# Kernel tuning notes

Hardware: AMD Instinct MI355X
Metric: run time of the kernel (lower is better)

The kernel has to match this reference:

```python
import jax, jax.numpy as jnp
import numpy as np
import math

N_HEAD = 16
N_HEAD_KV = 4
HEAD_DIM = 128
N_EMBD = 2048

def alibi_slopes(n_heads):
    def pow2_slopes(n):
        start = 2 ** (-2 ** (-(math.log2(n) - 3)))
        return [start * start ** i for i in range(n)]
    if math.log2(n_heads).is_integer():
        return jnp.array(pow2_slopes(n_heads), dtype=jnp.float32)
    closest = 2 ** math.floor(math.log2(n_heads))
    base = pow2_slopes(closest)
    if n_heads <= 2 * closest:
        s = base + base[0::2]
    else:
        s = base + base[0::2] + base[1::2]
    return jnp.array(s[:n_heads], dtype=jnp.float32)

def setup_inputs() -> dict:
    key = jax.random.key(0)
    ks = jax.random.split(key, 5)
    B, T, C = 2, 2048, N_EMBD
    kvdim = N_HEAD_KV * HEAD_DIM
    sc = 0.02
    return {
        "x": jax.random.normal(ks[0], (B, T, C), dtype=jnp.float32),
        "q_w": jax.random.normal(ks[1], (C, C), dtype=jnp.float32) * sc,
        "k_w": jax.random.normal(ks[2], (kvdim, C), dtype=jnp.float32) * sc,
        "v_w": jax.random.normal(ks[3], (kvdim, C), dtype=jnp.float32) * sc,
        "o_w": jax.random.normal(ks[4], (C, C), dtype=jnp.float32) * sc,
    }

def reference(x, q_w, k_w, v_w, o_w):
    B, T, C = x.shape
    H, Hkv, D = N_HEAD, N_HEAD_KV, HEAD_DIM
    # nan/inf sanitize (no-op for random inputs, kept for fidelity)
    x = jnp.nan_to_num(x, nan=0.0, posinf=10000.0, neginf=-10000.0)
    q = (x @ q_w.T).reshape(B, T, H, D).transpose(0, 2, 1, 3)      # [B,H,T,D]
    k = (x @ k_w.T).reshape(B, T, Hkv, D).transpose(0, 2, 1, 3)    # [B,Hkv,T,D]
    v = (x @ v_w.T).reshape(B, T, Hkv, D).transpose(0, 2, 1, 3)
    # repeat_interleave KV heads to H heads
    rep = H // Hkv
    k = jnp.repeat(k, rep, axis=1)
    v = jnp.repeat(v, rep, axis=1)
    scale = 1.0 / math.sqrt(D)
    att = jnp.einsum('bhqd,bhkd->bhqk', q, k) * scale
    att = jnp.clip(att, -10000.0, 10000.0)
    pos = jnp.arange(T)
    causal = jnp.where(pos[None, :] > pos[:, None], -jnp.inf, 0.0)  # [T,T]
    slopes = alibi_slopes(H)  # [H]
    rel = (pos[None, :] - pos[:, None]).astype(jnp.float32)         # [T,T]
    alibi = slopes[:, None, None] * rel[None]                        # [H,T,T]
    att = att + causal[None, None] + alibi[None]
    att = jax.nn.softmax(att.astype(jnp.float32), axis=-1).astype(q.dtype)
    y = jnp.einsum('bhqk,bhkd->bhqd', att, v)
    y = jnp.nan_to_num(y, nan=0.0, posinf=10000.0, neginf=-10000.0)
    y = y.transpose(0, 2, 1, 3).reshape(B, T, C)
    return y @ o_w.T
```

## Files before the change

kernel.cpp:

```cpp
#include <hip/hip_runtime.h>
#include <hip/hip_bf16.h>
#include <math.h>

#define SEQ   2048
#define EMBD  2048
#define NH    16
#define NKV   4
#define HD    128
#define NQKV  3072

typedef __attribute__((ext_vector_type(8))) short short8;
typedef __attribute__((ext_vector_type(4))) short short4v;
typedef __attribute__((ext_vector_type(4))) float floatx4;

static __device__ __forceinline__ short f2bf(float f) {
    union { float f; unsigned u; } cv; cv.f = f;
    unsigned u = cv.u;
    u += 0x7FFF + ((u >> 16) & 1);
    return (short)(u >> 16);
}

#define GL16(gsrc, ldst)                                                        \
    __builtin_amdgcn_global_load_lds(                                           \
        (const __attribute__((address_space(1))) void*)(gsrc),                  \
        (__attribute__((address_space(3))) void*)(ldst), 16, 0, 0)

static __device__ __forceinline__ int alibi_window(float slope2) {
    return (int)ceilf((42.0f / slope2 + 63.0f) * (1.0f / 64.0f));
}

__global__ void cvt_all(const float* __restrict__ x,  const float* __restrict__ qw,
                        const float* __restrict__ kw, const float* __restrict__ vw,
                        const float* __restrict__ ow,
                        short* __restrict__ xb, short* __restrict__ wall,
                        short* __restrict__ owb) {
    int i = blockIdx.x * blockDim.x + threadIdx.x;
    const float* src; short* dst; int off;
    if (i < 2097152)      { src = x;  dst = xb;             off = i; }
    else if (i < 3145728) { src = qw; dst = wall;           off = i - 2097152; }
    else if (i < 3407872) { src = kw; dst = wall + 4194304; off = i - 3145728; }
    else if (i < 3670016) { src = vw; dst = wall + 5242880; off = i - 3407872; }
    else                  { src = ow; dst = owb;            off = i - 3670016; }
    float4 v = ((const float4*)src)[off];
    float a[4] = {v.x, v.y, v.z, v.w};
    short4v o;
#pragma unroll
    for (int j = 0; j < 4; ++j) {
        float f = a[j];
        f = isnan(f) ? 0.0f : fminf(fmaxf(f, -10000.0f), 10000.0f);
        o[j] = f2bf(f);
    }
    ((short4v*)dst)[off] = o;
}

template<int MODE>
__global__ __launch_bounds__(256) void gemm_bt(
    const short* __restrict__ A, const short* __restrict__ W,
    float* __restrict__ Cout, int M, int N, int K,
    short* __restrict__ qb, short* __restrict__ kb, short* __restrict__ vb)
{
    __shared__ __align__(16) short sA[128 * 32];
    __shared__ __align__(16) short sB[128 * 32];

    const int tid  = threadIdx.x;
    const int lane = tid & 63;
    const int wv   = tid >> 6;
    const int wr   = wv >> 1, wc = wv & 1;
    const int lr   = lane & 15, lg = lane >> 4;
    const int bn   = blockIdx.x, bm = blockIdx.y;

    const short* gA[2]; const short* gB[2];
    short* lA[2]; short* lB[2];
#pragma unroll
    for (int s = 0; s < 2; ++s) {
        int chunk = wv * 128 + s * 64 + lane;
        int row = chunk >> 2, seg = chunk & 3;
        gA[s] = A + (size_t)(bm * 128 + row) * K + seg * 8;
        gB[s] = W + (size_t)(bn * 128 + row) * K + seg * 8;
        lA[s] = &sA[(wv * 128 + s * 64) * 8];
        lB[s] = &sB[(wv * 128 + s * 64) * 8];
    }

    floatx4 acc[4][4] = {};
    const int nkt = K / 32;
    for (int kt = 0; kt < nkt; ++kt) {
#pragma unroll
        for (int s = 0; s < 2; ++s) {
            GL16(gA[s] + kt * 32, lA[s]);
            GL16(gB[s] + kt * 32, lB[s]);
        }
        __syncthreads();

        short8 af[4], bfr[4];
#pragma unroll
        for (int i = 0; i < 4; ++i) {
            af[i]  = *(const short8*)&sA[(wr * 64 + i * 16 + lr) * 32 + lg * 8];
            bfr[i] = *(const short8*)&sB[(wc * 64 + i * 16 + lr) * 32 + lg * 8];
        }
#pragma unroll
        for (int i = 0; i < 4; ++i)
#pragma unroll
            for (int j = 0; j < 4; ++j)
                acc[i][j] = __builtin_amdgcn_mfma_f32_16x16x32_bf16(af[i], bfr[j], acc[i][j], 0, 0, 0);
        __syncthreads();
    }

    const float QSCALE = 0.08838834764831845f * 1.44269504f;
#pragma unroll
    for (int i = 0; i < 4; ++i)
#pragma unroll
        for (int j = 0; j < 4; ++j)
#pragma unroll
            for (int r = 0; r < 4; ++r) {
                int gm = bm * 128 + wr * 64 + i * 16 + lg * 4 + r;
                int gn = bn * 128 + wc * 64 + j * 16 + lr;
                float v = acc[i][j][r];
                if (MODE == 0) {
                    int b = gm >> 11, t = gm & (SEQ - 1);
                    if (gn < 2048) {
                        int h = gn >> 7, d = gn & 127;
                        qb[(((size_t)(b * NH + h)) * SEQ + t) * HD + d] = f2bf(v * QSCALE);
                    } else if (gn < 2560) {
                        int hk = (gn - 2048) >> 7, d = gn & 127;
                        kb[(((size_t)(b * NKV + hk)) * SEQ + t) * HD + d] = f2bf(v);
                    } else {
                        int hv = (gn - 2560) >> 7, d = gn & 127;
                        vb[(((size_t)(b * NKV + hv)) * HD + d) * SEQ + t] = f2bf(v);
                    }
                } else {
                    Cout[(size_t)gm * N + gn] = v;
                }
            }
}

__global__ __launch_bounds__(512, 4) void attn_fwd(
    const short* __restrict__ Q, const short* __restrict__ Kg,
    const short* __restrict__ VT, short* __restrict__ Y)
{
    __shared__ __align__(16) short sK[2][64 * 128];
    __shared__ __align__(16) short sV[128 * 64];
    __shared__ short Plds[8][16][72];

    const int tid  = threadIdx.x;
    const int wave = tid >> 6, lane = tid & 63;
    const int lr = lane & 15, lg = lane >> 4;
    const int bid = blockIdx.x;

    const int u = (bid & 1) ? (511 - (bid >> 1)) : (bid >> 1);
    const int p = u & 15, h = (u >> 4) & 15, b = u >> 8;
    const int hkv = h >> 2;
    const int qgw = 2 * p + (wave < 4 ? 1 : 0);

    const short* Qb = Q  +  ((size_t)(b * NH  + h  )) * SEQ * HD;
    const short* Kp = Kg +  ((size_t)(b * NKV + hkv)) * SEQ * HD;
    const short* Vp = VT +  ((size_t)(b * NKV + hkv)) * HD * SEQ;

    const float slope2 = exp2f(-0.5f * (float)(h + 1)) * 1.44269504f;
    const int W = alibi_window(slope2);
    const int thi = 2 * p + 1;
    int tlo = thi - W; if (tlo < 0) tlo = 0;

    const short* gK[2]; const short* gV[2];
    int lOff[2];
#pragma unroll
    for (int j = 0; j < 2; ++j) {
        int ck = wave * 128 + j * 64 + lane;
        int krow = ck >> 4, kseg = ck & 15;
        gK[j] = Kp + (size_t)krow * HD + (kseg ^ (krow & 7)) * 8;
        int vrow = ck >> 3, vseg = ck & 7;
        gV[j] = Vp + (size_t)vrow * SEQ + (vseg ^ (vrow & 7)) * 8;
        lOff[j] = (wave * 128 + j * 64) * 8;
    }

    float c_nt[4];
#pragma unroll
    for (int nt = 0; nt < 4; ++nt) c_nt[nt] = slope2 * (float)(nt * 16 + lr);

    const int q0 = qgw * 64 + (wave & 3) * 16;
    short8 qf[4];
#pragma unroll
    for (int cc = 0; cc < 4; ++cc)
        qf[cc] = *(const short8*)&Qb[(size_t)(q0 + lr) * HD + cc * 32 + lg * 8];

    floatx4 po[8] = {};
    float m[4], lsum[4];
#pragma unroll
    for (int r = 0; r < 4; ++r) { m[r] = -3.0e38f; lsum[r] = 0.0f; }

    int cur = 0;
#pragma unroll
    for (int j = 0; j < 2; ++j)
        GL16(gK[j] + (size_t)(thi << 6) * HD, &sK[0][0] + lOff[j]);
    __syncthreads();

#pragma unroll 1
    for (int t = thi; t >= tlo; --t) {
#pragma unroll
        for (int j = 0; j < 2; ++j)
            GL16(gV[j] + (t << 6), &sV[0] + lOff[j]);
        if (t > tlo) {
#pragma unroll
            for (int j = 0; j < 2; ++j)
                GL16(gK[j] + (size_t)((t - 1) << 6) * HD, &sK[cur ^ 1][0] + lOff[j]);
        }

        const bool active = (t <= qgw) && (t > qgw - W);
        const int kv0 = t << 6;

        if (active) {
            const short* kr = &sK[cur][0];
            floatx4 sf[4];
#pragma unroll
            for (int nt = 0; nt < 4; ++nt) {
                floatx4 sacc = {0.f, 0.f, 0.f, 0.f};
#pragma unroll
                for (int cc = 0; cc < 4; ++cc) {
                    int krow = nt * 16 + lr;
                    short8 kf = *(const short8*)&kr[krow * 128 + (((cc * 4 + lg) ^ (krow & 7)) * 8)];
                    sacc = __builtin_amdgcn_mfma_f32_16x16x32_bf16(qf[cc], kf, sacc, 0, 0, 0);
                }
                sf[nt] = sacc;
            }

            const float a2t = slope2 * (float)kv0;
            const bool masked = (t == qgw);
#pragma unroll
            for (int r = 0; r < 4; ++r) {
                const int qpos = q0 + lg * 4 + r;
                float sv[4];
#pragma unroll
                for (int nt = 0; nt < 4; ++nt)
                    sv[nt] = sf[nt][r] + a2t + c_nt[nt];
                if (masked) {
#pragma unroll
                    for (int nt = 0; nt < 4; ++nt) {
                        int kpos = kv0 + nt * 16 + lr;
                        if (kpos > qpos) sv[nt] = -3.0e38f;
                    }
                }
                bool over = (sv[0] > m[r]) | (sv[1] > m[r]) | (sv[2] > m[r]) | (sv[3] > m[r]);
                if (__any(over)) {
                    float mx = fmaxf(fmaxf(sv[0], sv[1]), fmaxf(sv[2], sv[3]));
#pragma unroll
                    for (int off = 1; off < 16; off <<= 1) mx = fmaxf(mx, __shfl_xor(mx, off));
                    float mn = fmaxf(m[r], mx);
                    float rs = exp2f(m[r] - mn);
                    lsum[r] *= rs;
#pragma unroll
                    for (int dt = 0; dt < 8; ++dt) po[dt][r] *= rs;
                    m[r] = mn;
                }
#pragma unroll
                for (int nt = 0; nt < 4; ++nt) {
                    float pp = exp2f(sv[nt] - m[r]);
                    lsum[r] += pp;
                    Plds[wave][lg * 4 + r][nt * 16 + lr] = f2bf(pp);
                }
            }
        }

        __syncthreads();

        if (active) {
            short8 pf0 = *(const short8*)&Plds[wave][lr][lg * 8];
            short8 pf1 = *(const short8*)&Plds[wave][lr][32 + lg * 8];
#pragma unroll
            for (int dt = 0; dt < 8; ++dt) {
                int vrow = dt * 16 + lr;
                short8 vf0 = *(const short8*)&sV[vrow * 64 + (((lg    ) ^ (vrow & 7)) * 8)];
                short8 vf1 = *(const short8*)&sV[vrow * 64 + (((lg + 4) ^ (vrow & 7)) * 8)];
                po[dt] = __builtin_amdgcn_mfma_f32_16x16x32_bf16(pf0, vf0, po[dt], 0, 0, 0);
                po[dt] = __builtin_amdgcn_mfma_f32_16x16x32_bf16(pf1, vf1, po[dt], 0, 0, 0);
            }
        }

        __syncthreads();
        cur ^= 1;
    }

#pragma unroll
    for (int r = 0; r < 4; ++r) {
        float sum = lsum[r];
#pragma unroll
        for (int off = 1; off < 16; off <<= 1) sum += __shfl_xor(sum, off);
        float inv = 1.0f / sum;
        int row = q0 + lg * 4 + r;
#pragma unroll
        for (int dt = 0; dt < 8; ++dt)
            Y[((size_t)(b * SEQ + row)) * EMBD + h * HD + dt * 16 + lr] = f2bf(po[dt][r] * inv);
    }
}

extern "C" void kernel_launch(void* const* d_in, const int* in_sizes, int n_in,
                              void* d_out, int out_size, void* d_ws, size_t ws_size,
                              hipStream_t stream) {
    const float* x   = (const float*)d_in[0];
    const float* q_w = (const float*)d_in[1];
    const float* k_w = (const float*)d_in[2];
    const float* v_w = (const float*)d_in[3];
    const float* o_w = (const float*)d_in[4];
    float* out = (float*)d_out;

    char* ws = (char*)d_ws;
    short* x_bf  = (short*)(ws);
    short* w_all = (short*)(ws + 16777216);
    short* o_wb  = (short*)(ws + 29360128);
    short* q_b   = (short*)(ws + 37748736);
    short* k_b   = (short*)(ws + 54525952);
    short* vT_b  = (short*)(ws + 58720256);
    short* y_b   = (short*)(ws + 62914560);

    cvt_all<<<18432, 256, 0, stream>>>(x, q_w, k_w, v_w, o_w, x_bf, w_all, o_wb);

    gemm_bt<0><<<dim3(NQKV / 128, 4096 / 128), 256, 0, stream>>>(
        x_bf, w_all, nullptr, 4096, NQKV, EMBD, q_b, k_b, vT_b);

    attn_fwd<<<512, 512, 0, stream>>>(q_b, k_b, vT_b, y_b);

    gemm_bt<1><<<dim3(EMBD / 128, 4096 / 128), 256, 0, stream>>>(
        y_b, o_wb, out, 4096, EMBD, EMBD, nullptr, nullptr, nullptr);
}
```

Measured before the change: 238.8 us.

## Double-buffer V tiles and replace full syncs with vmcnt-based waits

V tiles now get a second LDS buffer and are prefetched one iteration ahead together with K. The loop waits on outstanding global-to-LDS loads with explicit s_waitcnt vmcnt counts and raw s_barrier instead of __syncthreads. The P tile in LDS is XOR-swizzled with no padding, and the mid-loop barrier between softmax and PV is removed, since each wave only reads its own P slice. This adds LDS use, which may lower occupancy, and relies on hand-counted vmcnt values being correct.

```diff
diff --git a/kernel.cpp b/kernel.cpp
--- a/kernel.cpp
+++ b/kernel.cpp
@@ -138,8 +138,8 @@
     const short* __restrict__ VT, short* __restrict__ Y)
 {
     __shared__ __align__(16) short sK[2][64 * 128];
-    __shared__ __align__(16) short sV[128 * 64];
-    __shared__ short Plds[8][16][72];
+    __shared__ __align__(16) short sV[2][128 * 64];
+    __shared__ short Plds[8][16][64];
 
     const int tid  = threadIdx.x;
     const int wave = tid >> 6, lane = tid & 63;
@@ -181,6 +181,9 @@
 #pragma unroll
     for (int cc = 0; cc < 4; ++cc)
         qf[cc] = *(const short8*)&Qb[(size_t)(q0 + lr) * HD + cc * 32 + lg * 8];
+#pragma unroll
+    for (int cc = 0; cc < 4; ++cc)
+        asm volatile("" :: "v"(qf[cc]));
 
     floatx4 po[8] = {};
     float m[4], lsum[4];
@@ -189,20 +192,24 @@
 
     int cur = 0;
 #pragma unroll
-    for (int j = 0; j < 2; ++j)
+    for (int j = 0; j < 2; ++j) {
+        GL16(gV[j] + (thi << 6), &sV[0][0] + lOff[j]);
         GL16(gK[j] + (size_t)(thi << 6) * HD, &sK[0][0] + lOff[j]);
-    __syncthreads();
+    }
 
 #pragma unroll 1
     for (int t = thi; t >= tlo; --t) {
-#pragma unroll
-        for (int j = 0; j < 2; ++j)
-            GL16(gV[j] + (t << 6), &sV[0] + lOff[j]);
         if (t > tlo) {
 #pragma unroll
-            for (int j = 0; j < 2; ++j)
+            for (int j = 0; j < 2; ++j) {
+                GL16(gV[j] + ((t - 1) << 6), &sV[cur ^ 1][0] + lOff[j]);
                 GL16(gK[j] + (size_t)((t - 1) << 6) * HD, &sK[cur ^ 1][0] + lOff[j]);
+            }
+            asm volatile("s_waitcnt vmcnt(4)" ::: "memory");
+        } else {
+            asm volatile("s_waitcnt vmcnt(0)" ::: "memory");
         }
+        __builtin_amdgcn_s_barrier();
 
         const bool active = (t <= qgw) && (t > qgw - W);
         const int kv0 = t << 6;
@@ -227,6 +234,7 @@
 #pragma unroll
             for (int r = 0; r < 4; ++r) {
                 const int qpos = q0 + lg * 4 + r;
+                const int row = lg * 4 + r;
                 float sv[4];
 #pragma unroll
                 for (int nt = 0; nt < 4; ++nt)
@@ -254,27 +262,24 @@
                 for (int nt = 0; nt < 4; ++nt) {
                     float pp = exp2f(sv[nt] - m[r]);
                     lsum[r] += pp;
-                    Plds[wave][lg * 4 + r][nt * 16 + lr] = f2bf(pp);
-                }
-            }
-        }
-
-        __syncthreads();
-
-        if (active) {
-            short8 pf0 = *(const short8*)&Plds[wave][lr][lg * 8];
-            short8 pf1 = *(const short8*)&Plds[wave][lr][32 + lg * 8];
+                    Plds[wave][row][(((nt * 2 + (lr >> 3)) ^ (row & 7)) << 3) + (lr & 7)] = f2bf(pp);
+                }
+            }
+
+            short8 pf0 = *(const short8*)&Plds[wave][lr][((lg     ^ (lr & 7)) << 3)];
+            short8 pf1 = *(const short8*)&Plds[wave][lr][(((4 + lg) ^ (lr & 7)) << 3)];
+            const short* vr = &sV[cur][0];
 #pragma unroll
             for (int dt = 0; dt < 8; ++dt) {
                 int vrow = dt * 16 + lr;
-                short8 vf0 = *(const short8*)&sV[vrow * 64 + (((lg    ) ^ (vrow & 7)) * 8)];
-                short8 vf1 = *(const short8*)&sV[vrow * 64 + (((lg + 4) ^ (vrow & 7)) * 8)];
+                short8 vf0 = *(const short8*)&vr[vrow * 64 + (((lg    ) ^ (vrow & 7)) * 8)];
+                short8 vf1 = *(const short8*)&vr[vrow * 64 + (((lg + 4) ^ (vrow & 7)) * 8)];
                 po[dt] = __builtin_amdgcn_mfma_f32_16x16x32_bf16(pf0, vf0, po[dt], 0, 0, 0);
                 po[dt] = __builtin_amdgcn_mfma_f32_16x16x32_bf16(pf1, vf1, po[dt], 0, 0, 0);
             }
         }
 
-        __syncthreads();
+        __builtin_amdgcn_s_barrier();
         cur ^= 1;
     }
 
```

Measured after the change: 242.8 us. No clear change (+1.7%).

## Double GEMM K-tile with XOR-swizzled LDS and cost-sorted attention block scheduling

Applied to the files above, without the earlier changes.

The GEMM K-step grows from 32 to 64, with an XOR swizzle on the LDS layout meant to avoid bank conflicts, so there are half as many barriers per K. A small setup kernel ranks the attention work units by estimated ALiBi-window cost and writes a table. Attention blocks then read that table in a serpentine order so heavy units start first, which should balance load across CUs. This adds a tiny extra launch and doubles GEMM shared memory. The qtab table sits at the start of the workspace, overlapping x_bf, which has already been consumed by the QKV GEMM.

```diff
diff --git a/kernel.cpp b/kernel.cpp
--- a/kernel.cpp
+++ b/kernel.cpp
@@ -8,6 +8,7 @@
 #define NKV   4
 #define HD    128
 #define NQKV  3072
+#define NUNITS 512
 
 typedef __attribute__((ext_vector_type(8))) short short8;
 typedef __attribute__((ext_vector_type(4))) short short4v;
@@ -27,6 +28,12 @@
 
 static __device__ __forceinline__ int alibi_window(float slope2) {
     return (int)ceilf((42.0f / slope2 + 63.0f) * (1.0f / 64.0f));
+}
+
+static __device__ __forceinline__ int unit_cost(int h, int p) {
+    float slope2 = exp2f(-0.5f * (float)(h + 1)) * 1.44269504f;
+    int W = alibi_window(slope2);
+    return min(W + 1, 2 * p + 2);
 }
 
 __global__ void cvt_all(const float* __restrict__ x,  const float* __restrict__ qw,
@@ -53,14 +60,26 @@
     ((short4v*)dst)[off] = o;
 }
 
+__global__ void attn_setup(int* __restrict__ qtab) {
+    __shared__ int keys[NUNITS];
+    int i = threadIdx.x;
+    int hp = i >> 1;
+    int key = unit_cost(hp >> 4, hp & 15) * 1024 + i;
+    keys[i] = key;
+    __syncthreads();
+    int rank = 0;
+    for (int j = 0; j < NUNITS; ++j) rank += (keys[j] > key);
+    qtab[rank] = i;
+}
+
 template<int MODE>
 __global__ __launch_bounds__(256) void gemm_bt(
     const short* __restrict__ A, const short* __restrict__ W,
     float* __restrict__ Cout, int M, int N, int K,
     short* __restrict__ qb, short* __restrict__ kb, short* __restrict__ vb)
 {
-    __shared__ __align__(16) short sA[128 * 32];
-    __shared__ __align__(16) short sB[128 * 32];
+    __shared__ __align__(16) short sA[128 * 64];
+    __shared__ __align__(16) short sB[128 * 64];
 
     const int tid  = threadIdx.x;
     const int lane = tid & 63;
@@ -69,39 +88,45 @@
     const int lr   = lane & 15, lg = lane >> 4;
     const int bn   = blockIdx.x, bm = blockIdx.y;
 
-    const short* gA[2]; const short* gB[2];
-    short* lA[2]; short* lB[2];
-#pragma unroll
-    for (int s = 0; s < 2; ++s) {
-        int chunk = wv * 128 + s * 64 + lane;
-        int row = chunk >> 2, seg = chunk & 3;
-        gA[s] = A + (size_t)(bm * 128 + row) * K + seg * 8;
-        gB[s] = W + (size_t)(bn * 128 + row) * K + seg * 8;
-        lA[s] = &sA[(wv * 128 + s * 64) * 8];
-        lB[s] = &sB[(wv * 128 + s * 64) * 8];
+    const short* gA[4]; const short* gB[4];
+    short* lA[4]; short* lB[4];
+#pragma unroll
+    for (int s = 0; s < 4; ++s) {
+        int ck  = wv * 256 + s * 64 + lane;
+        int row = ck >> 3, seg = ck & 7;
+        int segSw = seg ^ (row & 7);
+        gA[s] = A + (size_t)(bm * 128 + row) * K + segSw * 8;
+        gB[s] = W + (size_t)(bn * 128 + row) * K + segSw * 8;
+        lA[s] = &sA[(wv * 256 + s * 64) * 8];
+        lB[s] = &sB[(wv * 256 + s * 64) * 8];
     }
 
     floatx4 acc[4][4] = {};
-    const int nkt = K / 32;
+    const int nkt = K / 64;
     for (int kt = 0; kt < nkt; ++kt) {
 #pragma unroll
-        for (int s = 0; s < 2; ++s) {
-            GL16(gA[s] + kt * 32, lA[s]);
-            GL16(gB[s] + kt * 32, lB[s]);
+        for (int s = 0; s < 4; ++s) {
+            GL16(gA[s] + kt * 64, lA[s]);
+            GL16(gB[s] + kt * 64, lB[s]);
         }
         __syncthreads();
 
-        short8 af[4], bfr[4];
-#pragma unroll
-        for (int i = 0; i < 4; ++i) {
-            af[i]  = *(const short8*)&sA[(wr * 64 + i * 16 + lr) * 32 + lg * 8];
-            bfr[i] = *(const short8*)&sB[(wc * 64 + i * 16 + lr) * 32 + lg * 8];
-        }
-#pragma unroll
-        for (int i = 0; i < 4; ++i)
-#pragma unroll
-            for (int j = 0; j < 4; ++j)
-                acc[i][j] = __builtin_amdgcn_mfma_f32_16x16x32_bf16(af[i], bfr[j], acc[i][j], 0, 0, 0);
+#pragma unroll
+        for (int ks = 0; ks < 2; ++ks) {
+            short8 af[4], bfr[4];
+#pragma unroll
+            for (int i = 0; i < 4; ++i) {
+                int ra = wr * 64 + i * 16 + lr;
+                int rb = wc * 64 + i * 16 + lr;
+                af[i]  = *(const short8*)&sA[ra * 64 + (((ks * 4 + lg) ^ (ra & 7)) * 8)];
+                bfr[i] = *(const short8*)&sB[rb * 64 + (((ks * 4 + lg) ^ (rb & 7)) * 8)];
+            }
+#pragma unroll
+            for (int i = 0; i < 4; ++i)
+#pragma unroll
+                for (int j = 0; j < 4; ++j)
+                    acc[i][j] = __builtin_amdgcn_mfma_f32_16x16x32_bf16(af[i], bfr[j], acc[i][j], 0, 0, 0);
+        }
         __syncthreads();
     }
 
@@ -135,7 +160,8 @@
 
 __global__ __launch_bounds__(512, 4) void attn_fwd(
     const short* __restrict__ Q, const short* __restrict__ Kg,
-    const short* __restrict__ VT, short* __restrict__ Y)
+    const short* __restrict__ VT, short* __restrict__ Y,
+    const int* __restrict__ qtab)
 {
     __shared__ __align__(16) short sK[2][64 * 128];
     __shared__ __align__(16) short sV[128 * 64];
@@ -146,8 +172,10 @@
     const int lr = lane & 15, lg = lane >> 4;
     const int bid = blockIdx.x;
 
-    const int u = (bid & 1) ? (511 - (bid >> 1)) : (bid >> 1);
-    const int p = u & 15, h = (u >> 4) & 15, b = u >> 8;
+    const int rank = (bid < 256) ? bid : (767 - bid);
+    const int uu = qtab[rank];
+    const int b = uu & 1, hp = uu >> 1;
+    const int h = hp >> 4, p = hp & 15;
     const int hkv = h >> 2;
     const int qgw = 2 * p + (wave < 4 ? 1 : 0);
 
@@ -309,13 +337,15 @@
     short* k_b   = (short*)(ws + 54525952);
     short* vT_b  = (short*)(ws + 58720256);
     short* y_b   = (short*)(ws + 62914560);
+    int*   qtab  = (int*)(ws);
 
     cvt_all<<<18432, 256, 0, stream>>>(x, q_w, k_w, v_w, o_w, x_bf, w_all, o_wb);
 
     gemm_bt<0><<<dim3(NQKV / 128, 4096 / 128), 256, 0, stream>>>(
         x_bf, w_all, nullptr, 4096, NQKV, EMBD, q_b, k_b, vT_b);
 
-    attn_fwd<<<512, 512, 0, stream>>>(q_b, k_b, vT_b, y_b);
+    attn_setup<<<1, NUNITS, 0, stream>>>(qtab);
+    attn_fwd<<<512, 512, 0, stream>>>(q_b, k_b, vT_b, y_b, qtab);
 
     gemm_bt<1><<<dim3(EMBD / 128, 4096 / 128), 256, 0, stream>>>(
         y_b, o_wb, out, 4096, EMBD, EMBD, nullptr, nullptr, nullptr);
```

New measurement: 212.4 us. -11.0%, faster.
